# Performance work log

Measured on AMD Instinct MI355X. Metric: run time of the kernel, lower is better.

## Reference

```python
import jax, jax.numpy as jnp
import numpy as np

EMBED_DIM = 768
NUM_HEADS = 12
HEAD_DIM = EMBED_DIM // NUM_HEADS


def setup_inputs() -> dict:
    key = jax.random.key(0)
    ks = jax.random.split(key, 9)
    B, N, C = 4, 2048, EMBED_DIM
    s = 1.0 / np.sqrt(C)
    x = jax.random.normal(ks[0], (B, N, C), dtype=jnp.float32)
    Wq = jax.random.normal(ks[1], (C, C), dtype=jnp.float32) * s
    bq = jnp.zeros((C,), dtype=jnp.float32)
    Wk = jax.random.normal(ks[2], (C, C), dtype=jnp.float32) * s
    bk = jnp.zeros((C,), dtype=jnp.float32)
    Wv = jax.random.normal(ks[3], (C, C), dtype=jnp.float32) * s
    bv = jnp.zeros((C,), dtype=jnp.float32)
    Wo = jax.random.normal(ks[4], (C, C), dtype=jnp.float32) * s
    bo = jnp.zeros((C,), dtype=jnp.float32)
    return {"x": x, "Wq": Wq, "bq": bq, "Wk": Wk, "bk": bk,
            "Wv": Wv, "bv": bv, "Wo": Wo, "bo": bo}


def reference(x, Wq, bq, Wk, bk, Wv, bv, Wo, bo):
    # Dropout in eval mode (identity), matching module.eval().
    B, N, C = x.shape
    H, D = NUM_HEADS, HEAD_DIM
    scale = D ** -0.5

    def split_heads(t):  # [B,N,C] -> [B,H,N,D]
        return t.reshape(B, N, H, D).transpose(0, 2, 1, 3)

    q = split_heads(x @ Wq.T + bq)
    k = split_heads(x @ Wk.T + bk)
    v = split_heads(x @ Wv.T + bv)

    attn = jnp.einsum('bhnd,bhmd->bhnm', q, k) * scale  # [B,H,N,N]
    attn = jax.nn.softmax(attn, axis=-1)
    out = jnp.einsum('bhnm,bhmd->bhnd', attn, v)        # [B,H,N,D]
    out = out.transpose(0, 2, 1, 3).reshape(B, N, C)
    return out @ Wo.T + bo
```

## Files before the change

kernel.cpp:

```cpp
#include <hip/hip_runtime.h>
#include <math.h>

#define CDIM 768
#define NHEADS 12
#define HDIM 64
#define BATCH 4
#define SEQ 2048
#define MTOT (BATCH*SEQ)
#define NQKV (3*CDIM)
#define QROWS 128
#define VTILE 4096

typedef __attribute__((ext_vector_type(8))) short bf16x8;
typedef __attribute__((ext_vector_type(4))) float f32x4;
typedef unsigned short u16;
typedef unsigned int u32;

#define ASYNC16(gsrc, ldst) \
  __builtin_amdgcn_global_load_lds((const __attribute__((address_space(1))) void*)(gsrc), \
                                   (__attribute__((address_space(3))) void*)(ldst), 16, 0, 0)

__device__ inline u16 f2b(float x) {
    unsigned int u = __float_as_uint(x);
    return (u16)((u + 0x7fffu + ((u >> 16) & 1u)) >> 16);
}
__device__ inline u32 prnd(float x) { return __float_as_uint(x) + 0x8000u; }

#define XBLK (MTOT*CDIM/1024)
#define WBLK (CDIM*CDIM/1024)
__global__ __launch_bounds__(256)
void prep_kern(const float* __restrict__ x,
               const float* __restrict__ Wq, const float* __restrict__ Wk,
               const float* __restrict__ Wv, const float* __restrict__ Wo,
               const float* __restrict__ bq, const float* __restrict__ bk,
               const float* __restrict__ bv,
               u16* __restrict__ xb, u16* __restrict__ wqkv, u16* __restrict__ wob,
               float* __restrict__ bcat)
{
    int bx = blockIdx.x, tid = threadIdx.x;
    if (bx < XBLK) {
        int i = (bx * 256 + tid) * 4;
        float4 v = *(const float4*)(x + i);
        ushort4 o;
        o.x = f2b(v.x); o.y = f2b(v.y); o.z = f2b(v.z); o.w = f2b(v.w);
        *(ushort4*)(xb + i) = o;
    } else if (bx < XBLK + 4*WBLK) {
        int z = (bx - XBLK) / WBLK;
        int blk = (bx - XBLK) % WBLK;
        const float* src = (z == 0) ? Wq : (z == 1) ? Wk : (z == 2) ? Wv : Wo;
        u16* dst = (z == 3) ? wob : wqkv + (size_t)z * CDIM * CDIM;
        int i = (blk * 256 + tid) * 4;
        float4 v = *(const float4*)(src + i);
        ushort4 o;
        o.x = f2b(v.x); o.y = f2b(v.y); o.z = f2b(v.z); o.w = f2b(v.w);
        *(ushort4*)(dst + i) = o;
    } else {
        int i = (bx - XBLK - 4*WBLK) * 256 + tid;
        if (i < CDIM) bcat[i] = bq[i];
        else if (i < 2*CDIM) bcat[i] = bk[i - CDIM];
        else if (i < 3*CDIM) bcat[i] = bv[i - 2*CDIM];
    }
}

template<int OUTF32, int VFRAG>
__global__ __launch_bounds__(256)
void gemm_bf16(const u16* __restrict__ A, const u16* __restrict__ B,
               const float* __restrict__ bias, void* __restrict__ Y,
               u16* __restrict__ Vt,
               int N, int K, int qn, float qscale)
{
    __shared__ __align__(16) u16 As[2][128*64];
    __shared__ __align__(16) u16 Bs[2][128*64];
    const int tid = threadIdx.x;
    const int nwg = gridDim.x * gridDim.y;
    const int fid = blockIdx.y * gridDim.x + blockIdx.x;
    const int swz = (fid & 7) * (nwg >> 3) + (fid >> 3);
    const int m0 = (swz / gridDim.x) * 128, n0 = (swz % gridDim.x) * 128;
    const int wid = tid >> 6, lane = tid & 63;
    const int wm = (wid & 1) * 64, wn = (wid >> 1) * 64;
    const int l15 = lane & 15, quad = lane >> 4;

    f32x4 acc[4][4];
    #pragma unroll
    for (int i = 0; i < 4; ++i)
        #pragma unroll
        for (int j = 0; j < 4; ++j)
            #pragma unroll
            for (int r = 0; r < 4; ++r) acc[i][j][r] = 0.f;

    auto stage = [&](int buf, int t) {
        int k0 = t * 64;
        #pragma unroll
        for (int r = 0; r < 4; ++r) {
            int li = r*256 + tid;
            int row = li >> 3, c = li & 7;
            int gc = c ^ (row & 7);
            ASYNC16(A + (size_t)(m0 + row) * K + k0 + gc*8, &As[buf][li*8]);
            ASYNC16(B + (size_t)(n0 + row) * K + k0 + gc*8, &Bs[buf][li*8]);
        }
    };

    const int NT = K / 64;
    stage(0, 0);
    __syncthreads();

    for (int t = 0; t < NT; ++t) {
        const int bufc = t & 1;
        if (t + 1 < NT) stage(bufc ^ 1, t + 1);
        #pragma unroll
        for (int kk = 0; kk < 2; ++kk) {
            bf16x8 a[4], b[4];
            #pragma unroll
            for (int i = 0; i < 4; ++i) {
                int m = wm + i*16 + l15;
                int ca = (kk*4 + quad) ^ (m & 7);
                a[i] = *(const bf16x8*)&As[bufc][m*64 + ca*8];
                int n = wn + i*16 + l15;
                int cbx = (kk*4 + quad) ^ (n & 7);
                b[i] = *(const bf16x8*)&Bs[bufc][n*64 + cbx*8];
            }
            #pragma unroll
            for (int i = 0; i < 4; ++i)
                #pragma unroll
                for (int j = 0; j < 4; ++j)
                    acc[i][j] = __builtin_amdgcn_mfma_f32_16x16x32_bf16(a[i], b[j], acc[i][j], 0, 0, 0);
        }
        __syncthreads();
    }

    if (VFRAG && n0 >= 2*CDIM) {
        #pragma unroll
        for (int i = 0; i < 4; ++i) {
            int gm = m0 + wm + i*16 + quad*4;
            int bb = gm >> 11;
            int kt = (gm & 2047) >> 6;
            int t  = i >> 1;
            int wj = (i & 1) * 4;
            #pragma unroll
            for (int j = 0; j < 4; ++j) {
                int gn = n0 + wn + j*16 + l15;
                float bv = bias[gn];
                int d = gn - 2*CDIM;
                int h = d >> 6, jd = (d & 63) >> 4;
                int bh = bb * NHEADS + h;
                u32 p0 = prnd(acc[i][j][0] + bv);
                u32 p1 = prnd(acc[i][j][1] + bv);
                u32 p2 = prnd(acc[i][j][2] + bv);
                u32 p3 = prnd(acc[i][j][3] + bv);
                uint2 st;
                st.x = __builtin_amdgcn_perm(p1, p0, 0x07060302u);
                st.y = __builtin_amdgcn_perm(p3, p2, 0x07060302u);
                *(uint2*)(Vt + ((size_t)(bh*32 + kt))*VTILE
                             + (size_t)((t*4 + jd)*64 + lane)*8 + wj) = st;
            }
        }
    } else {
        #pragma unroll
        for (int i = 0; i < 4; ++i) {
            #pragma unroll
            for (int j = 0; j < 4; ++j) {
                int gn = n0 + wn + j*16 + l15;
                float bv = bias[gn];
                float sc = (gn < qn) ? qscale : 1.0f;
                #pragma unroll
                for (int r = 0; r < 4; ++r) {
                    int gm = m0 + wm + i*16 + quad*4 + r;
                    float v = (acc[i][j][r] + bv) * sc;
                    if (OUTF32) ((float*)Y)[(size_t)gm * N + gn] = v;
                    else        ((u16*)Y)[(size_t)gm * N + gn] = f2b(v);
                }
            }
        }
    }
}

__global__ __launch_bounds__(256, 3)
void attn_mfma(const u16* __restrict__ QK, const u16* __restrict__ Vt,
               u16* __restrict__ Oa)
{
    __shared__ __align__(16) u16 Ks[2][64*64];
    __shared__ __align__(16) u16 Vls[2][2048];

    const int tid = threadIdx.x;
    const int wid = tid >> 6, lane = tid & 63;
    const int l15 = lane & 15, quad = lane >> 4;
    const int fid = blockIdx.y * gridDim.x + blockIdx.x;
    const int swz = (fid & 7) * 96 + (fid >> 3);
    const int qt = swz & 15, bh = swz >> 4;
    const int b = bh / NHEADS, h = bh % NHEADS;

    const u16* Qg  = QK + ((size_t)(b*SEQ + qt*QROWS)) * NQKV + h*HDIM;
    const u16* Kg0 = QK + ((size_t)(b*SEQ)) * NQKV + CDIM + h*HDIM;
    const u16* Vg  = Vt + (size_t)bh * 32 * VTILE;

    #pragma unroll
    for (int r = 0; r < 2; ++r) {
        int li = r*256 + tid, row = li >> 3, c = li & 7, gc = c ^ (row & 7);
        ASYNC16(Kg0 + (size_t)row * NQKV + gc*8, &Ks[0][li*8]);
    }
    ASYNC16(Vg + tid*8, &Vls[0][tid*8]);

    bf16x8 qf[2][2];
    #pragma unroll
    for (int mb = 0; mb < 2; ++mb)
        #pragma unroll
        for (int kk = 0; kk < 2; ++kk)
            qf[mb][kk] = *(const bf16x8*)(Qg + (size_t)(wid*32 + mb*16 + l15) * NQKV + kk*32 + quad*8);

    const bf16x8 ONES8 = { (short)0x3F80, (short)0x3F80, (short)0x3F80, (short)0x3F80,
                           (short)0x3F80, (short)0x3F80, (short)0x3F80, (short)0x3F80 };
    const f32x4 ZERO4 = { 0.f, 0.f, 0.f, 0.f };

    f32x4 o[2][4];
    #pragma unroll
    for (int mb = 0; mb < 2; ++mb)
        #pragma unroll
        for (int j = 0; j < 4; ++j)
            #pragma unroll
            for (int r = 0; r < 4; ++r) o[mb][j][r] = 0.f;
    f32x4 ll[2];
    #pragma unroll
    for (int mb = 0; mb < 2; ++mb)
        #pragma unroll
        for (int r = 0; r < 4; ++r) ll[mb][r] = 0.f;

    __syncthreads();

    auto body = [&](int kt, int cbuf, int nbuf) {
        if (kt + 1 < SEQ/64) {
            #pragma unroll
            for (int r = 0; r < 2; ++r) {
                int li = r*256 + tid, row = li >> 3, c = li & 7, gc = c ^ (row & 7);
                ASYNC16(Kg0 + (size_t)((kt+1)*64 + row) * NQKV + gc*8, &Ks[nbuf][li*8]);
            }
            ASYNC16(Vg + (size_t)(kt+1) * VTILE + tid*8, &Vls[nbuf][tid*8]);
        }

        bf16x8 vf[2][4];
        #pragma unroll
        for (int jd = 0; jd < 4; ++jd) {
            vf[0][jd] = *(const bf16x8*)&Vls[cbuf][(size_t)(jd*64 + lane)*8];
            vf[1][jd] = *(const bf16x8*)(Vg + (size_t)kt * VTILE
                                         + (size_t)((4 + jd)*64 + lane)*8);
        }

        f32x4 s[2][4];
        __builtin_amdgcn_s_setprio(1);
        #pragma unroll
        for (int j = 0; j < 4; ++j) {
            int kr = j*16 + l15;
            int ck = quad ^ (kr & 7);
            bf16x8 ak = *(const bf16x8*)&Ks[cbuf][kr*64 + ck*8];
            #pragma unroll
            for (int mb = 0; mb < 2; ++mb)
                s[mb][j] = __builtin_amdgcn_mfma_f32_16x16x32_bf16(ak, qf[mb][0], ZERO4, 0, 0, 0);
        }
        #pragma unroll
        for (int j = 0; j < 4; ++j) {
            int kr = j*16 + l15;
            int ck = (4 + quad) ^ (kr & 7);
            bf16x8 ak = *(const bf16x8*)&Ks[cbuf][kr*64 + ck*8];
            #pragma unroll
            for (int mb = 0; mb < 2; ++mb)
                s[mb][j] = __builtin_amdgcn_mfma_f32_16x16x32_bf16(ak, qf[mb][1], s[mb][j], 0, 0, 0);
        }
        __builtin_amdgcn_s_setprio(0);

        bf16x8 pf[2][2];
        #pragma unroll
        for (int mb = 0; mb < 2; ++mb)
            #pragma unroll
            for (int t = 0; t < 2; ++t) {
                u32 a0 = prnd(__builtin_amdgcn_exp2f(s[mb][2*t][0]));
                u32 a1 = prnd(__builtin_amdgcn_exp2f(s[mb][2*t][1]));
                u32 a2 = prnd(__builtin_amdgcn_exp2f(s[mb][2*t][2]));
                u32 a3 = prnd(__builtin_amdgcn_exp2f(s[mb][2*t][3]));
                u32 b0 = prnd(__builtin_amdgcn_exp2f(s[mb][2*t+1][0]));
                u32 b1 = prnd(__builtin_amdgcn_exp2f(s[mb][2*t+1][1]));
                u32 b2 = prnd(__builtin_amdgcn_exp2f(s[mb][2*t+1][2]));
                u32 b3 = prnd(__builtin_amdgcn_exp2f(s[mb][2*t+1][3]));
                union { uint4 u; bf16x8 v; } cst;
                cst.u.x = __builtin_amdgcn_perm(a1, a0, 0x07060302u);
                cst.u.y = __builtin_amdgcn_perm(a3, a2, 0x07060302u);
                cst.u.z = __builtin_amdgcn_perm(b1, b0, 0x07060302u);
                cst.u.w = __builtin_amdgcn_perm(b3, b2, 0x07060302u);
                pf[mb][t] = cst.v;
            }

        __builtin_amdgcn_s_setprio(1);
        #pragma unroll
        for (int t = 0; t < 2; ++t) {
            #pragma unroll
            for (int jd = 0; jd < 4; ++jd) {
                #pragma unroll
                for (int mb = 0; mb < 2; ++mb)
                    o[mb][jd] = __builtin_amdgcn_mfma_f32_16x16x32_bf16(pf[mb][t], vf[t][jd], o[mb][jd], 0, 0, 0);
            }
            #pragma unroll
            for (int mb = 0; mb < 2; ++mb)
                ll[mb] = __builtin_amdgcn_mfma_f32_16x16x32_bf16(pf[mb][t], ONES8, ll[mb], 0, 0, 0);
        }
        __builtin_amdgcn_s_setprio(0);
        __syncthreads();
    };

    for (int kt = 0; kt < SEQ/64; kt += 2) {
        body(kt,   0, 1);
        body(kt+1, 1, 0);
    }

    u16* Og = Oa + ((size_t)(b*SEQ + qt*QROWS)) * CDIM + h*HDIM;
    #pragma unroll
    for (int mb = 0; mb < 2; ++mb) {
        #pragma unroll
        for (int r = 0; r < 4; ++r) {
            float inv = 1.f / ll[mb][r];
            int row = wid*32 + mb*16 + quad*4 + r;
            #pragma unroll
            for (int jd = 0; jd < 4; ++jd)
                Og[(size_t)row * CDIM + jd*16 + l15] = f2b(o[mb][jd][r] * inv);
        }
    }
}

extern "C" void kernel_launch(void* const* d_in, const int* in_sizes, int n_in,
                              void* d_out, int out_size, void* d_ws, size_t ws_size,
                              hipStream_t stream)
{
    const float* x  = (const float*)d_in[0];
    const float* Wq = (const float*)d_in[1];
    const float* bq = (const float*)d_in[2];
    const float* Wk = (const float*)d_in[3];
    const float* bk = (const float*)d_in[4];
    const float* Wv = (const float*)d_in[5];
    const float* bv = (const float*)d_in[6];
    const float* Wo = (const float*)d_in[7];
    const float* bo = (const float*)d_in[8];

    unsigned char* ws = (unsigned char*)d_ws;
    u16* xb   = (u16*)ws;  ws += (size_t)MTOT * CDIM * 2;
    u16* wqkv = (u16*)ws;  ws += (size_t)NQKV * CDIM * 2;
    u16* wob  = (u16*)ws;  ws += (size_t)CDIM * CDIM * 2;
    float* bcat = (float*)ws; ws += (size_t)NQKV * 4;
    u16* qkv  = (u16*)ws;  ws += (size_t)MTOT * NQKV * 2;
    u16* vt   = (u16*)ws;  ws += (size_t)BATCH*NHEADS*32*VTILE * 2;
    u16* ao   = (u16*)ws;

    prep_kern<<<XBLK + 4*WBLK + 9, 256, 0, stream>>>(x, Wq, Wk, Wv, Wo, bq, bk, bv,
                                                     xb, wqkv, wob, bcat);

    gemm_bf16<0,1><<<dim3(NQKV/128, MTOT/128), 256, 0, stream>>>(xb, wqkv, bcat, qkv, vt, NQKV, CDIM, CDIM, 0.18033688f);
    attn_mfma<<<dim3(SEQ/QROWS, BATCH*NHEADS), 256, 0, stream>>>(qkv, vt, ao);
    gemm_bf16<1,0><<<dim3(CDIM/128, MTOT/128), 256, 0, stream>>>(ao, wob, bo, (float*)d_out, nullptr, CDIM, CDIM, 0, 1.0f);
}
```

Measured before the change: 210.7 us.

## Software-pipeline attention loop: overlap QK^T of next tile with PV of previous

Restructures the attention key loop so that each step computes the S=QK^T MFMAs for the current key tile and then performs exp2/pack and PV MFMAs for the previous tile, using ping-pong register sets for scores and V fragments. This aims to hide the latency of the score MFMAs and the exp computation behind independent work. The extra live registers force launch bounds down from 3 to 2 blocks per SM, trading occupancy for instruction-level overlap.

```diff
diff --git a/kernel.cpp b/kernel.cpp
--- a/kernel.cpp
+++ b/kernel.cpp
@@ -174,7 +174,7 @@
     }
 }
 
-__global__ __launch_bounds__(256, 3)
+__global__ __launch_bounds__(256, 2)
 void attn_mfma(const u16* __restrict__ QK, const u16* __restrict__ Vt,
                u16* __restrict__ Oa)
 {
@@ -224,61 +224,25 @@
         #pragma unroll
         for (int r = 0; r < 4; ++r) ll[mb][r] = 0.f;
 
+    f32x4 sA[2][4], sB[2][4];
+    bf16x8 vfA[2][4], vfB[2][4];
+
     __syncthreads();
 
-    auto body = [&](int kt, int cbuf, int nbuf) {
-        if (kt + 1 < SEQ/64) {
-            #pragma unroll
-            for (int r = 0; r < 2; ++r) {
-                int li = r*256 + tid, row = li >> 3, c = li & 7, gc = c ^ (row & 7);
-                ASYNC16(Kg0 + (size_t)((kt+1)*64 + row) * NQKV + gc*8, &Ks[nbuf][li*8]);
-            }
-            ASYNC16(Vg + (size_t)(kt+1) * VTILE + tid*8, &Vls[nbuf][tid*8]);
-        }
-
-        bf16x8 vf[2][4];
-        #pragma unroll
-        for (int jd = 0; jd < 4; ++jd) {
-            vf[0][jd] = *(const bf16x8*)&Vls[cbuf][(size_t)(jd*64 + lane)*8];
-            vf[1][jd] = *(const bf16x8*)(Vg + (size_t)kt * VTILE
-                                         + (size_t)((4 + jd)*64 + lane)*8);
-        }
-
-        f32x4 s[2][4];
-        __builtin_amdgcn_s_setprio(1);
-        #pragma unroll
-        for (int j = 0; j < 4; ++j) {
-            int kr = j*16 + l15;
-            int ck = quad ^ (kr & 7);
-            bf16x8 ak = *(const bf16x8*)&Ks[cbuf][kr*64 + ck*8];
-            #pragma unroll
-            for (int mb = 0; mb < 2; ++mb)
-                s[mb][j] = __builtin_amdgcn_mfma_f32_16x16x32_bf16(ak, qf[mb][0], ZERO4, 0, 0, 0);
-        }
-        #pragma unroll
-        for (int j = 0; j < 4; ++j) {
-            int kr = j*16 + l15;
-            int ck = (4 + quad) ^ (kr & 7);
-            bf16x8 ak = *(const bf16x8*)&Ks[cbuf][kr*64 + ck*8];
-            #pragma unroll
-            for (int mb = 0; mb < 2; ++mb)
-                s[mb][j] = __builtin_amdgcn_mfma_f32_16x16x32_bf16(ak, qf[mb][1], s[mb][j], 0, 0, 0);
-        }
-        __builtin_amdgcn_s_setprio(0);
-
+    auto finish = [&](f32x4 (&sP)[2][4], bf16x8 (&vfP)[2][4]) {
         bf16x8 pf[2][2];
         #pragma unroll
         for (int mb = 0; mb < 2; ++mb)
             #pragma unroll
             for (int t = 0; t < 2; ++t) {
-                u32 a0 = prnd(__builtin_amdgcn_exp2f(s[mb][2*t][0]));
-                u32 a1 = prnd(__builtin_amdgcn_exp2f(s[mb][2*t][1]));
-                u32 a2 = prnd(__builtin_amdgcn_exp2f(s[mb][2*t][2]));
-                u32 a3 = prnd(__builtin_amdgcn_exp2f(s[mb][2*t][3]));
-                u32 b0 = prnd(__builtin_amdgcn_exp2f(s[mb][2*t+1][0]));
-                u32 b1 = prnd(__builtin_amdgcn_exp2f(s[mb][2*t+1][1]));
-                u32 b2 = prnd(__builtin_amdgcn_exp2f(s[mb][2*t+1][2]));
-                u32 b3 = prnd(__builtin_amdgcn_exp2f(s[mb][2*t+1][3]));
+                u32 a0 = prnd(__builtin_amdgcn_exp2f(sP[mb][2*t][0]));
+                u32 a1 = prnd(__builtin_amdgcn_exp2f(sP[mb][2*t][1]));
+                u32 a2 = prnd(__builtin_amdgcn_exp2f(sP[mb][2*t][2]));
+                u32 a3 = prnd(__builtin_amdgcn_exp2f(sP[mb][2*t][3]));
+                u32 b0 = prnd(__builtin_amdgcn_exp2f(sP[mb][2*t+1][0]));
+                u32 b1 = prnd(__builtin_amdgcn_exp2f(sP[mb][2*t+1][1]));
+                u32 b2 = prnd(__builtin_amdgcn_exp2f(sP[mb][2*t+1][2]));
+                u32 b3 = prnd(__builtin_amdgcn_exp2f(sP[mb][2*t+1][3]));
                 union { uint4 u; bf16x8 v; } cst;
                 cst.u.x = __builtin_amdgcn_perm(a1, a0, 0x07060302u);
                 cst.u.y = __builtin_amdgcn_perm(a3, a2, 0x07060302u);
@@ -286,7 +250,6 @@
                 cst.u.w = __builtin_amdgcn_perm(b3, b2, 0x07060302u);
                 pf[mb][t] = cst.v;
             }
-
         __builtin_amdgcn_s_setprio(1);
         #pragma unroll
         for (int t = 0; t < 2; ++t) {
@@ -294,20 +257,67 @@
             for (int jd = 0; jd < 4; ++jd) {
                 #pragma unroll
                 for (int mb = 0; mb < 2; ++mb)
-                    o[mb][jd] = __builtin_amdgcn_mfma_f32_16x16x32_bf16(pf[mb][t], vf[t][jd], o[mb][jd], 0, 0, 0);
+                    o[mb][jd] = __builtin_amdgcn_mfma_f32_16x16x32_bf16(pf[mb][t], vfP[t][jd], o[mb][jd], 0, 0, 0);
             }
             #pragma unroll
             for (int mb = 0; mb < 2; ++mb)
                 ll[mb] = __builtin_amdgcn_mfma_f32_16x16x32_bf16(pf[mb][t], ONES8, ll[mb], 0, 0, 0);
         }
         __builtin_amdgcn_s_setprio(0);
+    };
+
+    auto step = [&](int kt, int cbuf, int nbuf,
+                    f32x4 (&sP)[2][4], bf16x8 (&vfP)[2][4],
+                    f32x4 (&sC)[2][4], bf16x8 (&vfC)[2][4], bool first) {
+        if (kt + 1 < SEQ/64) {
+            #pragma unroll
+            for (int r = 0; r < 2; ++r) {
+                int li = r*256 + tid, row = li >> 3, c = li & 7, gc = c ^ (row & 7);
+                ASYNC16(Kg0 + (size_t)((kt+1)*64 + row) * NQKV + gc*8, &Ks[nbuf][li*8]);
+            }
+            ASYNC16(Vg + (size_t)(kt+1) * VTILE + tid*8, &Vls[nbuf][tid*8]);
+        }
+
+        #pragma unroll
+        for (int jd = 0; jd < 4; ++jd) {
+            vfC[0][jd] = *(const bf16x8*)&Vls[cbuf][(size_t)(jd*64 + lane)*8];
+            vfC[1][jd] = *(const bf16x8*)(Vg + (size_t)kt * VTILE
+                                          + (size_t)((4 + jd)*64 + lane)*8);
+        }
+
+        __builtin_amdgcn_s_setprio(1);
+        #pragma unroll
+        for (int j = 0; j < 4; ++j) {
+            int kr = j*16 + l15;
+            int ck = quad ^ (kr & 7);
+            bf16x8 ak = *(const bf16x8*)&Ks[cbuf][kr*64 + ck*8];
+            #pragma unroll
+            for (int mb = 0; mb < 2; ++mb)
+                sC[mb][j] = __builtin_amdgcn_mfma_f32_16x16x32_bf16(ak, qf[mb][0], ZERO4, 0, 0, 0);
+        }
+        #pragma unroll
+        for (int j = 0; j < 4; ++j) {
+            int kr = j*16 + l15;
+            int ck = (4 + quad) ^ (kr & 7);
+            bf16x8 ak = *(const bf16x8*)&Ks[cbuf][kr*64 + ck*8];
+            #pragma unroll
+            for (int mb = 0; mb < 2; ++mb)
+                sC[mb][j] = __builtin_amdgcn_mfma_f32_16x16x32_bf16(ak, qf[mb][1], sC[mb][j], 0, 0, 0);
+        }
+        __builtin_amdgcn_s_setprio(0);
+
+        if (!first) finish(sP, vfP);
+
         __syncthreads();
     };
 
-    for (int kt = 0; kt < SEQ/64; kt += 2) {
-        body(kt,   0, 1);
-        body(kt+1, 1, 0);
-    }
+    step(0, 0, 1, sB, vfB, sA, vfA, true);
+    for (int kt = 1; kt < 31; kt += 2) {
+        step(kt,   1, 0, sA, vfA, sB, vfB, false);
+        step(kt+1, 0, 1, sB, vfB, sA, vfA, false);
+    }
+    step(31, 1, 0, sA, vfA, sB, vfB, false);
+    finish(sB, vfB);
 
     u16* Og = Oa + ((size_t)(b*SEQ + qt*QROWS)) * CDIM + h*HDIM;
     #pragma unroll
```

Result: slower. 227.3 us (+7.9%).

## Stage two K/V tiles per barrier in attention loop

Applied to the files above, without the earlier changes.

The attention kernel's LDS double buffer now holds two 64-key K/V tiles per stage instead of one. Each loop iteration prefetches the next pair of tiles asynchronously, processes the current pair, then hits a single __syncthreads. This halves the block-wide barriers and gives each prefetch more compute to hide behind. The cost is twice the shared memory per block (about 48KB), which may limit how many blocks fit on a CU alongside the launch-bounds target.

```diff
diff --git a/kernel.cpp b/kernel.cpp
--- a/kernel.cpp
+++ b/kernel.cpp
@@ -178,8 +178,8 @@
 void attn_mfma(const u16* __restrict__ QK, const u16* __restrict__ Vt,
                u16* __restrict__ Oa)
 {
-    __shared__ __align__(16) u16 Ks[2][64*64];
-    __shared__ __align__(16) u16 Vls[2][2048];
+    __shared__ __align__(16) u16 Ks[2][2][64*64];
+    __shared__ __align__(16) u16 Vls[2][2][2048];
 
     const int tid = threadIdx.x;
     const int wid = tid >> 6, lane = tid & 63;
@@ -193,12 +193,19 @@
     const u16* Kg0 = QK + ((size_t)(b*SEQ)) * NQKV + CDIM + h*HDIM;
     const u16* Vg  = Vt + (size_t)bh * 32 * VTILE;
 
-    #pragma unroll
-    for (int r = 0; r < 2; ++r) {
-        int li = r*256 + tid, row = li >> 3, c = li & 7, gc = c ^ (row & 7);
-        ASYNC16(Kg0 + (size_t)row * NQKV + gc*8, &Ks[0][li*8]);
-    }
-    ASYNC16(Vg + tid*8, &Vls[0][tid*8]);
+    auto stage2 = [&](int wp, int kt) {
+        #pragma unroll
+        for (int u = 0; u < 2; ++u) {
+            #pragma unroll
+            for (int r = 0; r < 2; ++r) {
+                int li = r*256 + tid, row = li >> 3, c = li & 7, gc = c ^ (row & 7);
+                ASYNC16(Kg0 + (size_t)((kt+u)*64 + row) * NQKV + gc*8, &Ks[wp][u][li*8]);
+            }
+            ASYNC16(Vg + (size_t)(kt+u) * VTILE + tid*8, &Vls[wp][u][tid*8]);
+        }
+    };
+
+    stage2(0, 0);
 
     bf16x8 qf[2][2];
     #pragma unroll
@@ -226,20 +233,11 @@
 
     __syncthreads();
 
-    auto body = [&](int kt, int cbuf, int nbuf) {
-        if (kt + 1 < SEQ/64) {
-            #pragma unroll
-            for (int r = 0; r < 2; ++r) {
-                int li = r*256 + tid, row = li >> 3, c = li & 7, gc = c ^ (row & 7);
-                ASYNC16(Kg0 + (size_t)((kt+1)*64 + row) * NQKV + gc*8, &Ks[nbuf][li*8]);
-            }
-            ASYNC16(Vg + (size_t)(kt+1) * VTILE + tid*8, &Vls[nbuf][tid*8]);
-        }
-
+    auto body = [&](int kt, int rp, int u) {
         bf16x8 vf[2][4];
         #pragma unroll
         for (int jd = 0; jd < 4; ++jd) {
-            vf[0][jd] = *(const bf16x8*)&Vls[cbuf][(size_t)(jd*64 + lane)*8];
+            vf[0][jd] = *(const bf16x8*)&Vls[rp][u][(size_t)(jd*64 + lane)*8];
             vf[1][jd] = *(const bf16x8*)(Vg + (size_t)kt * VTILE
                                          + (size_t)((4 + jd)*64 + lane)*8);
         }
@@ -250,7 +248,7 @@
         for (int j = 0; j < 4; ++j) {
             int kr = j*16 + l15;
             int ck = quad ^ (kr & 7);
-            bf16x8 ak = *(const bf16x8*)&Ks[cbuf][kr*64 + ck*8];
+            bf16x8 ak = *(const bf16x8*)&Ks[rp][u][kr*64 + ck*8];
             #pragma unroll
             for (int mb = 0; mb < 2; ++mb)
                 s[mb][j] = __builtin_amdgcn_mfma_f32_16x16x32_bf16(ak, qf[mb][0], ZERO4, 0, 0, 0);
@@ -259,7 +257,7 @@
         for (int j = 0; j < 4; ++j) {
             int kr = j*16 + l15;
             int ck = (4 + quad) ^ (kr & 7);
-            bf16x8 ak = *(const bf16x8*)&Ks[cbuf][kr*64 + ck*8];
+            bf16x8 ak = *(const bf16x8*)&Ks[rp][u][kr*64 + ck*8];
             #pragma unroll
             for (int mb = 0; mb < 2; ++mb)
                 s[mb][j] = __builtin_amdgcn_mfma_f32_16x16x32_bf16(ak, qf[mb][1], s[mb][j], 0, 0, 0);
@@ -301,12 +299,14 @@
                 ll[mb] = __builtin_amdgcn_mfma_f32_16x16x32_bf16(pf[mb][t], ONES8, ll[mb], 0, 0, 0);
         }
         __builtin_amdgcn_s_setprio(0);
+    };
+
+    for (int s = 0; s < 16; ++s) {
+        const int rp = s & 1, wp = rp ^ 1;
+        if (s < 15) stage2(wp, 2*s + 2);
+        body(2*s,     rp, 0);
+        body(2*s + 1, rp, 1);
         __syncthreads();
-    };
-
-    for (int kt = 0; kt < SEQ/64; kt += 2) {
-        body(kt,   0, 1);
-        body(kt+1, 1, 0);
     }
 
     u16* Og = Oa + ((size_t)(b*SEQ + qt*QROWS)) * CDIM + h*HDIM;
```

Measured after the change: 209.6 us, median of 2. Within noise of the previous version (-0.5%).
